# Kernel optimization log

Hardware: AMD Instinct MI355X
Metric: run time of the kernel (lower is better)

## Reference

```python
import math
import jax, jax.numpy as jnp
import numpy as np

S, B, H, D = 2048, 1, 16, 128  # seq, batch, heads, head_dim (hard-coded in source)
COEFF = 1.0  # layer_num = 1
NORM_FACTOR = math.sqrt(2048 / 16) * COEFF  # sqrt(HIDDEN/NUM_HEADS) * coeff


def setup_inputs() -> dict:
    key = jax.random.key(0)
    k1, k2, k3, k4, k5 = jax.random.split(key, 5)
    query_layer = jax.random.normal(k1, (S, B, H, D), dtype=jnp.float32)
    key_layer = jax.random.normal(k2, (S, B, H, D), dtype=jnp.float32)
    value_layer = jax.random.normal(k3, (S, B, H, D), dtype=jnp.float32)
    # causal mask, True = masked (Megatron convention)
    attention_mask = jnp.triu(jnp.ones((S, S), dtype=bool), k=1)[None, None]
    # per-head SVD right-singular-vector matrices (orthonormal-ish; random here)
    svd_qk = jax.random.normal(k4, (H, D, D), dtype=jnp.float32) / math.sqrt(D)
    svd_v = jax.random.normal(k5, (H, D, D), dtype=jnp.float32) / math.sqrt(D)
    return {"query_layer": query_layer, "key_layer": key_layer,
            "value_layer": value_layer, "attention_mask": attention_mask,
            "svd_qk": svd_qk, "svd_v": svd_v}


def reference(query_layer, key_layer, value_layer, attention_mask, svd_qk, svd_v):
    # q/k/v: [S, 1, H, D] -> project each head through its SVD matrix
    q = jnp.einsum('shd,hde->hse', query_layer[:, 0], svd_qk)  # [H,S,D]
    k = jnp.einsum('shd,hde->hse', key_layer[:, 0], svd_qk)    # [H,S,D]
    # qk_drop = 0 -> h_mask zeroing of columns is a no-op (faithfully skipped)
    scores = jnp.einsum('hqe,hke->hqk', q, k) / NORM_FACTOR    # [H,S,S]
    mask = attention_mask[0, 0]                                 # [S,S] bool
    scores = jnp.where(mask, jnp.float32(-10000.0), scores)
    # FusedScaleMaskSoftmax: scale by coeff, re-mask, softmax
    scaled = jnp.where(mask, jnp.float32(-10000.0), scores * COEFF)
    probs = jax.nn.softmax(scaled, axis=-1)                     # [H,S,S]
    # attention dropout is identity in eval mode
    v = jnp.einsum('shd,hde->hse', value_layer[:, 0], svd_v)    # [H,S,D]
    # vlinear_drop = 0 -> column zeroing is a no-op
    ctx = jnp.einsum('hqk,hke->qhe', probs, v)                  # [S,H,D]
    return ctx.reshape(S, B, H * D)                             # [S,1,2048]
```

## Files before the change

kernel.cpp:

```cpp
#include <hip/hip_runtime.h>
#include <hip/hip_bf16.h>
#include <math.h>

#define S_LEN 2048
#define NHEAD 16
#define DHEAD 128

typedef __attribute__((ext_vector_type(8)))  _Float16 f16x8;
typedef __attribute__((ext_vector_type(4)))  _Float16 f16x4;
typedef __attribute__((ext_vector_type(2)))  _Float16 f16x2;
typedef __attribute__((ext_vector_type(4)))  float    f32x4;
typedef __attribute__((ext_vector_type(16))) float    f32x16;

__device__ __forceinline__ void permswap(unsigned &a, unsigned &b) {
    asm volatile("v_permlane32_swap_b32 %0, %1" : "+v"(a), "+v"(b));
}

__global__ __launch_bounds__(256) void transpose_w_kernel(
    const float* __restrict__ w_qk, const float* __restrict__ w_v,
    _Float16* __restrict__ wqk_t, _Float16* __restrict__ wv_t)
{
    __shared__ float tile[32][33];
    const int mat = blockIdx.z;
    const int h   = blockIdx.y;
    const int t0  = blockIdx.x;
    const int dt  = (t0 >> 2) * 32;
    const int et  = (t0 & 3) * 32;
    const float* src = (mat ? w_v : w_qk) + (size_t)h * DHEAD * DHEAD;
    _Float16*   dst = (mat ? wv_t : wqk_t) + (size_t)h * DHEAD * DHEAD;
    const int tx = threadIdx.x & 31, ty = threadIdx.x >> 5;
#pragma unroll
    for (int k = 0; k < 4; ++k)
        tile[ty + 8 * k][tx] = src[(size_t)(dt + ty + 8 * k) * DHEAD + et + tx];
    __syncthreads();
#pragma unroll
    for (int k = 0; k < 4; ++k)
        dst[(size_t)(et + ty + 8 * k) * DHEAD + dt + tx] = (_Float16)tile[tx][ty + 8 * k];
}

__global__ __launch_bounds__(256) void proj_kernel(
    const float* __restrict__ q_in, const float* __restrict__ k_in,
    const float* __restrict__ v_in,
    const _Float16* __restrict__ wqk_t, const _Float16* __restrict__ wv_t,
    _Float16* __restrict__ Qp, _Float16* __restrict__ Kp, _Float16* __restrict__ Vt)
{
    const int h   = blockIdx.x >> 5;
    const int rb  = blockIdx.x & 31;
    const int wv  = threadIdx.x >> 6;
    const int lane = threadIdx.x & 63;
    const int r16 = lane & 15;
    const int kg  = lane >> 4;
    const int s_base = rb * 64 + wv * 16;
    const int s_row  = s_base + r16;
    const float INV_NORM = 0.08838834764831845f;

    f16x8 aq[4], ak[4], av[4];
    {
        const float* qr = q_in + ((size_t)s_row * NHEAD + h) * DHEAD;
        const float* kr = k_in + ((size_t)s_row * NHEAD + h) * DHEAD;
        const float* vr = v_in + ((size_t)s_row * NHEAD + h) * DHEAD;
#pragma unroll
        for (int kb = 0; kb < 4; ++kb) {
            const int d0 = kb * 32 + kg * 8;
            const f32x4 q0 = *(const f32x4*)(qr + d0), q1 = *(const f32x4*)(qr + d0 + 4);
            const f32x4 k0 = *(const f32x4*)(kr + d0), k1 = *(const f32x4*)(kr + d0 + 4);
            const f32x4 v0 = *(const f32x4*)(vr + d0), v1 = *(const f32x4*)(vr + d0 + 4);
#pragma unroll
            for (int i = 0; i < 4; ++i) {
                aq[kb][i] = (_Float16)q0[i];  aq[kb][i + 4] = (_Float16)q1[i];
                ak[kb][i] = (_Float16)k0[i];  ak[kb][i + 4] = (_Float16)k1[i];
                av[kb][i] = (_Float16)v0[i];  av[kb][i + 4] = (_Float16)v1[i];
            }
        }
    }

    const _Float16* wq_h = wqk_t + (size_t)h * DHEAD * DHEAD;
    const _Float16* wv_h = wv_t  + (size_t)h * DHEAD * DHEAD;

#pragma unroll 2
    for (int cb = 0; cb < 8; ++cb) {
        f32x4 accq = {0.f, 0.f, 0.f, 0.f};
        f32x4 acck = {0.f, 0.f, 0.f, 0.f};
        f32x4 accv = {0.f, 0.f, 0.f, 0.f};
        const int c = cb * 16 + r16;
#pragma unroll
        for (int kb = 0; kb < 4; ++kb) {
            const f16x8 bqk = *(const f16x8*)(wq_h + (size_t)c * DHEAD + kb * 32 + kg * 8);
            const f16x8 bv  = *(const f16x8*)(wv_h + (size_t)c * DHEAD + kb * 32 + kg * 8);
            accq = __builtin_amdgcn_mfma_f32_16x16x32_f16(aq[kb], bqk, accq, 0, 0, 0);
            acck = __builtin_amdgcn_mfma_f32_16x16x32_f16(ak[kb], bqk, acck, 0, 0, 0);
            accv = __builtin_amdgcn_mfma_f32_16x16x32_f16(av[kb], bv,  accv, 0, 0, 0);
        }
#pragma unroll
        for (int j = 0; j < 4; ++j) {
            const int sr = s_base + kg * 4 + j;
            Qp[((size_t)h * S_LEN + sr) * DHEAD + c] = (_Float16)(accq[j] * INV_NORM);
            Kp[((size_t)h * S_LEN + sr) * DHEAD + c] = (_Float16)acck[j];
        }
        f16x4 vvv;
#pragma unroll
        for (int j = 0; j < 4; ++j) vvv[j] = (_Float16)accv[j];
        *(f16x4*)(Vt + ((size_t)h * DHEAD + c) * S_LEN + s_base + kg * 4) = vvv;
    }
}

__global__ __launch_bounds__(512, 2) void attn_kernel(
    const _Float16* __restrict__ Qp, const _Float16* __restrict__ Kp,
    const _Float16* __restrict__ Vt, float* __restrict__ out)
{
    __shared__ _Float16 obuf[4][32][132];
    __shared__ float    mlbuf[4][2][32];

    const int h    = blockIdx.y;
    const int w    = threadIdx.x >> 6;
    const int lane = threadIdx.x & 63;
    const int q    = lane & 31;
    const int hi   = lane >> 5;

    const int qsub = w & 1;
    const int role = (w >> 1) & 1;
    const int tsel = w >> 2;
    const int t    = tsel ? (31 - blockIdx.x) : blockIdx.x;
    const int pairid = qsub + tsel * 2;
    const int q0w  = t * 64 + qsub * 32;
    const int jmax = 2 * t + 1 + qsub;
    const int q_abs = q0w + q;

    const _Float16* qbase = Qp + ((size_t)h * S_LEN + q0w) * DHEAD;
    const _Float16* kbase = Kp + (size_t)h * S_LEN * DHEAD;
    const _Float16* vbase = Vt + (size_t)h * DHEAD * S_LEN;

    const int lqk = q * DHEAD + hi * 8;
    const int lv  = q * S_LEN + hi * 8;

    f16x8 qf[8];
#pragma unroll
    for (int m = 0; m < 8; ++m)
        qf[m] = *(const f16x8*)(qbase + lqk + m * 16);

    f32x16 acc[4];
#pragma unroll
    for (int e = 0; e < 4; ++e)
#pragma unroll
        for (int i = 0; i < 16; ++i) acc[e][i] = 0.f;

    float m_run = -1e30f, l_run = 0.f;

    for (int j = role; j < jmax; j += 2) {
        const int kv0 = j * 32;

        const _Float16* kp = kbase + (size_t)kv0 * DHEAD + lqk;
        f16x8 kf[8];
#pragma unroll
        for (int m = 0; m < 8; ++m)
            kf[m] = *(const f16x8*)(kp + m * 16);

        f32x16 s0, s1;
#pragma unroll
        for (int i = 0; i < 16; ++i) { s0[i] = 0.f; s1[i] = 0.f; }
#pragma unroll
        for (int m = 0; m < 8; m += 2) {
            s0 = __builtin_amdgcn_mfma_f32_32x32x16_f16(kf[m],     qf[m],     s0, 0, 0, 0);
            s1 = __builtin_amdgcn_mfma_f32_32x32x16_f16(kf[m + 1], qf[m + 1], s1, 0, 0, 0);
        }

        f16x8 vf[8];
#pragma unroll
        for (int e = 0; e < 4; ++e) {
            const _Float16* vp = vbase + (size_t)e * 32 * S_LEN + lv + kv0;
            vf[2 * e]     = *(const f16x8*)(vp);
            vf[2 * e + 1] = *(const f16x8*)(vp + 16);
        }

        f32x16 sv = s0 + s1;

        if (kv0 == q0w) {
#pragma unroll
            for (int i = 0; i < 16; ++i) {
                const int krel = (i & 3) + 8 * (i >> 2) + 4 * hi;
                if (kv0 + krel > q_abs) sv[i] = -1e30f;
            }
        }

        float t0 = fmaxf(sv[0], sv[1]),  t1 = fmaxf(sv[2], sv[3]);
        float t2 = fmaxf(sv[4], sv[5]),  t3 = fmaxf(sv[6], sv[7]);
        float t4 = fmaxf(sv[8], sv[9]),  t5 = fmaxf(sv[10], sv[11]);
        float t6 = fmaxf(sv[12], sv[13]), t7 = fmaxf(sv[14], sv[15]);
        t0 = fmaxf(t0, t1); t2 = fmaxf(t2, t3); t4 = fmaxf(t4, t5); t6 = fmaxf(t6, t7);
        float tm = fmaxf(fmaxf(t0, t2), fmaxf(t4, t6));
        tm = fmaxf(tm, __shfl_xor(tm, 32, 64));

        const float mnew = fmaxf(m_run, tm);
        if (__any(tm > m_run)) {
            const float corr = __expf(m_run - mnew);
            l_run *= corr;
#pragma unroll
            for (int e = 0; e < 4; ++e)
#pragma unroll
                for (int i = 0; i < 16; ++i) acc[e][i] *= corr;
            m_run = mnew;
        }

#pragma unroll
        for (int i = 0; i < 16; ++i) sv[i] = __expf(sv[i] - m_run);
        float r0 = (sv[0] + sv[1]) + (sv[2] + sv[3]);
        float r1 = (sv[4] + sv[5]) + (sv[6] + sv[7]);
        float r2 = (sv[8] + sv[9]) + (sv[10] + sv[11]);
        float r3 = (sv[12] + sv[13]) + (sv[14] + sv[15]);
        float rs = (r0 + r1) + (r2 + r3);
        rs += __shfl_xor(rs, 32, 64);
        l_run += rs;

        unsigned u0 = __builtin_bit_cast(unsigned, __builtin_amdgcn_cvt_pkrtz(sv[0],  sv[1]));
        unsigned u1 = __builtin_bit_cast(unsigned, __builtin_amdgcn_cvt_pkrtz(sv[2],  sv[3]));
        unsigned u2 = __builtin_bit_cast(unsigned, __builtin_amdgcn_cvt_pkrtz(sv[4],  sv[5]));
        unsigned u3 = __builtin_bit_cast(unsigned, __builtin_amdgcn_cvt_pkrtz(sv[6],  sv[7]));
        unsigned u4 = __builtin_bit_cast(unsigned, __builtin_amdgcn_cvt_pkrtz(sv[8],  sv[9]));
        unsigned u5 = __builtin_bit_cast(unsigned, __builtin_amdgcn_cvt_pkrtz(sv[10], sv[11]));
        unsigned u6 = __builtin_bit_cast(unsigned, __builtin_amdgcn_cvt_pkrtz(sv[12], sv[13]));
        unsigned u7 = __builtin_bit_cast(unsigned, __builtin_amdgcn_cvt_pkrtz(sv[14], sv[15]));
        permswap(u0, u2); permswap(u1, u3);
        permswap(u4, u6); permswap(u5, u7);
        union uf8 { unsigned w[4]; f16x8 v; };
        uf8 p0; p0.w[0] = u0; p0.w[1] = u1; p0.w[2] = u2; p0.w[3] = u3;
        uf8 p1; p1.w[0] = u4; p1.w[1] = u5; p1.w[2] = u6; p1.w[3] = u7;

#pragma unroll
        for (int e = 0; e < 4; ++e) {
            acc[e] = __builtin_amdgcn_mfma_f32_32x32x16_f16(vf[2 * e],     p0.v, acc[e], 0, 0, 0);
            acc[e] = __builtin_amdgcn_mfma_f32_32x32x16_f16(vf[2 * e + 1], p1.v, acc[e], 0, 0, 0);
        }
    }

    if (role) {
        if (hi == 0) { mlbuf[pairid][0][q] = m_run; mlbuf[pairid][1][q] = l_run; }
#pragma unroll
        for (int e = 0; e < 4; ++e)
#pragma unroll
            for (int i = 0; i < 16; ++i) {
                const int erow = e * 32 + (i & 3) + 8 * (i >> 2) + 4 * hi;
                obuf[pairid][q][erow] = (_Float16)acc[e][i];
            }
    }
    __syncthreads();
    if (!role) {
        const float mb = mlbuf[pairid][0][q];
        const float lb = mlbuf[pairid][1][q];
        const float ms = fmaxf(m_run, mb);
        const float ca = __expf(m_run - ms);
        const float cb = __expf(mb - ms);
        const float rinv = 1.0f / (l_run * ca + lb * cb);
        float* orow = out + (size_t)q_abs * (NHEAD * DHEAD) + h * DHEAD;
#pragma unroll
        for (int e = 0; e < 4; ++e) {
#pragma unroll
            for (int g = 0; g < 4; ++g) {
                f32x4 vv;
#pragma unroll
                for (int c = 0; c < 4; ++c) {
                    const int i = g * 4 + c;
                    const int erow = e * 32 + 8 * g + 4 * hi + c;
                    vv[c] = (acc[e][i] * ca + (float)obuf[pairid][q][erow] * cb) * rinv;
                }
                *(f32x4*)(orow + e * 32 + 8 * g + 4 * hi) = vv;
            }
        }
    }
}

extern "C" void kernel_launch(void* const* d_in, const int* in_sizes, int n_in,
                              void* d_out, int out_size, void* d_ws, size_t ws_size,
                              hipStream_t stream) {
    const float* q_in = (const float*)d_in[0];
    const float* k_in = (const float*)d_in[1];
    const float* v_in = (const float*)d_in[2];
    const float* w_qk = (const float*)d_in[4];
    const float* w_v  = (const float*)d_in[5];
    float* out = (float*)d_out;

    const size_t mat_elems = (size_t)NHEAD * S_LEN * DHEAD;
    const size_t w_elems   = (size_t)NHEAD * DHEAD * DHEAD;
    _Float16* Qp   = (_Float16*)d_ws;
    _Float16* Kp   = Qp + mat_elems;
    _Float16* Vt   = Kp + mat_elems;
    _Float16* Wqkt = Vt + mat_elems;
    _Float16* Wvt  = Wqkt + w_elems;

    transpose_w_kernel<<<dim3(16, NHEAD, 2), dim3(256), 0, stream>>>(w_qk, w_v, Wqkt, Wvt);
    proj_kernel<<<dim3(NHEAD * 32), dim3(256), 0, stream>>>(q_in, k_in, v_in, Wqkt, Wvt, Qp, Kp, Vt);
    attn_kernel<<<dim3(16, NHEAD), dim3(512), 0, stream>>>(Qp, Kp, Vt, out);
}
```

Baseline: 105.0 us.

## Restructure attention into 16-row query tiles using 16x16x32 MFMA and K prefetch

```diff
diff --git a/kernel.cpp b/kernel.cpp
--- a/kernel.cpp
+++ b/kernel.cpp
@@ -8,13 +8,7 @@
 
 typedef __attribute__((ext_vector_type(8)))  _Float16 f16x8;
 typedef __attribute__((ext_vector_type(4)))  _Float16 f16x4;
-typedef __attribute__((ext_vector_type(2)))  _Float16 f16x2;
 typedef __attribute__((ext_vector_type(4)))  float    f32x4;
-typedef __attribute__((ext_vector_type(16))) float    f32x16;
-
-__device__ __forceinline__ void permswap(unsigned &a, unsigned &b) {
-    asm volatile("v_permlane32_swap_b32 %0, %1" : "+v"(a), "+v"(b));
-}
 
 __global__ __launch_bounds__(256) void transpose_w_kernel(
     const float* __restrict__ w_qk, const float* __restrict__ w_v,
@@ -52,7 +46,7 @@
     const int kg  = lane >> 4;
     const int s_base = rb * 64 + wv * 16;
     const int s_row  = s_base + r16;
-    const float INV_NORM = 0.08838834764831845f;
+    const float INV_NORM = 0.12752211758f;
 
     f16x8 aq[4], ak[4], av[4];
     {
@@ -104,166 +98,157 @@
     }
 }
 
-__global__ __launch_bounds__(512, 2) void attn_kernel(
+__global__ __launch_bounds__(512, 4) void attn_kernel(
     const _Float16* __restrict__ Qp, const _Float16* __restrict__ Kp,
     const _Float16* __restrict__ Vt, float* __restrict__ out)
 {
-    __shared__ _Float16 obuf[4][32][132];
-    __shared__ float    mlbuf[4][2][32];
+    __shared__ _Float16 obuf[4][16][136];
+    __shared__ float    mlbuf[4][2][16];
 
     const int h    = blockIdx.y;
     const int w    = threadIdx.x >> 6;
     const int lane = threadIdx.x & 63;
-    const int q    = lane & 31;
-    const int hi   = lane >> 5;
-
-    const int qsub = w & 1;
-    const int role = (w >> 1) & 1;
+    const int r16  = lane & 15;
+    const int kg   = lane >> 4;
+
     const int tsel = w >> 2;
-    const int t    = tsel ? (31 - blockIdx.x) : blockIdx.x;
-    const int pairid = qsub + tsel * 2;
-    const int q0w  = t * 64 + qsub * 32;
-    const int jmax = 2 * t + 1 + qsub;
-    const int q_abs = q0w + q;
-
-    const _Float16* qbase = Qp + ((size_t)h * S_LEN + q0w) * DHEAD;
+    const int qsub = (w >> 1) & 1;
+    const int role = w & 1;
+    const int t    = tsel ? (63 - blockIdx.x) : blockIdx.x;
+    const int mg   = tsel * 2 + qsub;
+    const int q0w  = t * 32 + qsub * 16;
+    const int jmax = t + 1;
+    const int q_abs = q0w + r16;
+
     const _Float16* kbase = Kp + (size_t)h * S_LEN * DHEAD;
     const _Float16* vbase = Vt + (size_t)h * DHEAD * S_LEN;
 
-    const int lqk = q * DHEAD + hi * 8;
-    const int lv  = q * S_LEN + hi * 8;
-
-    f16x8 qf[8];
-#pragma unroll
-    for (int m = 0; m < 8; ++m)
-        qf[m] = *(const f16x8*)(qbase + lqk + m * 16);
-
-    f32x16 acc[4];
-#pragma unroll
-    for (int e = 0; e < 4; ++e)
-#pragma unroll
-        for (int i = 0; i < 16; ++i) acc[e][i] = 0.f;
-
+    f16x8 qf[4];
+    {
+        const _Float16* qp = Qp + ((size_t)h * S_LEN + q_abs) * DHEAD + kg * 8;
+#pragma unroll
+        for (int st = 0; st < 4; ++st) qf[st] = *(const f16x8*)(qp + st * 32);
+    }
+
+    f32x4 acc[8];
+#pragma unroll
+    for (int eb = 0; eb < 8; ++eb) acc[eb] = (f32x4){0.f, 0.f, 0.f, 0.f};
     float m_run = -1e30f, l_run = 0.f;
 
-    for (int j = role; j < jmax; j += 2) {
+    const int lkoff = r16 * DHEAD + kg * 8;
+
+    auto loadK = [&](f16x8* kf, int j) {
+        const _Float16* kp = kbase + (size_t)(j * 32) * DHEAD + lkoff;
+#pragma unroll
+        for (int b = 0; b < 2; ++b)
+#pragma unroll
+            for (int st = 0; st < 4; ++st)
+                kf[b * 4 + st] = *(const f16x8*)(kp + b * 16 * DHEAD + st * 32);
+    };
+
+    auto tile = [&](const f16x8* kf, int j) {
         const int kv0 = j * 32;
-
-        const _Float16* kp = kbase + (size_t)kv0 * DHEAD + lqk;
-        f16x8 kf[8];
-#pragma unroll
-        for (int m = 0; m < 8; ++m)
-            kf[m] = *(const f16x8*)(kp + m * 16);
-
-        f32x16 s0, s1;
-#pragma unroll
-        for (int i = 0; i < 16; ++i) { s0[i] = 0.f; s1[i] = 0.f; }
-#pragma unroll
-        for (int m = 0; m < 8; m += 2) {
-            s0 = __builtin_amdgcn_mfma_f32_32x32x16_f16(kf[m],     qf[m],     s0, 0, 0, 0);
-            s1 = __builtin_amdgcn_mfma_f32_32x32x16_f16(kf[m + 1], qf[m + 1], s1, 0, 0, 0);
-        }
-
+        f32x4 s0 = {0.f, 0.f, 0.f, 0.f}, s1 = {0.f, 0.f, 0.f, 0.f};
+#pragma unroll
+        for (int st = 0; st < 4; ++st) {
+            s0 = __builtin_amdgcn_mfma_f32_16x16x32_f16(kf[st],     qf[st], s0, 0, 0, 0);
+            s1 = __builtin_amdgcn_mfma_f32_16x16x32_f16(kf[4 + st], qf[st], s1, 0, 0, 0);
+        }
         f16x8 vf[8];
 #pragma unroll
-        for (int e = 0; e < 4; ++e) {
-            const _Float16* vp = vbase + (size_t)e * 32 * S_LEN + lv + kv0;
-            vf[2 * e]     = *(const f16x8*)(vp);
-            vf[2 * e + 1] = *(const f16x8*)(vp + 16);
-        }
-
-        f32x16 sv = s0 + s1;
-
-        if (kv0 == q0w) {
-#pragma unroll
-            for (int i = 0; i < 16; ++i) {
-                const int krel = (i & 3) + 8 * (i >> 2) + 4 * hi;
+        for (int eb = 0; eb < 8; ++eb) {
+            const _Float16* vp = vbase + (size_t)(eb * 16 + r16) * S_LEN + kv0 + kg * 4;
+            union { f16x4 h[2]; f16x8 v; } uu;
+            uu.h[0] = *(const f16x4*)(vp);
+            uu.h[1] = *(const f16x4*)(vp + 16);
+            vf[eb] = uu.v;
+        }
+
+        float sv[8];
+#pragma unroll
+        for (int i = 0; i < 4; ++i) { sv[i] = s0[i]; sv[4 + i] = s1[i]; }
+
+        if (j == t) {
+#pragma unroll
+            for (int i = 0; i < 8; ++i) {
+                const int krel = ((i >> 2) << 4) + kg * 4 + (i & 3);
                 if (kv0 + krel > q_abs) sv[i] = -1e30f;
             }
         }
 
-        float t0 = fmaxf(sv[0], sv[1]),  t1 = fmaxf(sv[2], sv[3]);
-        float t2 = fmaxf(sv[4], sv[5]),  t3 = fmaxf(sv[6], sv[7]);
-        float t4 = fmaxf(sv[8], sv[9]),  t5 = fmaxf(sv[10], sv[11]);
-        float t6 = fmaxf(sv[12], sv[13]), t7 = fmaxf(sv[14], sv[15]);
-        t0 = fmaxf(t0, t1); t2 = fmaxf(t2, t3); t4 = fmaxf(t4, t5); t6 = fmaxf(t6, t7);
-        float tm = fmaxf(fmaxf(t0, t2), fmaxf(t4, t6));
+        float t0 = fmaxf(sv[0], sv[1]), t1 = fmaxf(sv[2], sv[3]);
+        float t2 = fmaxf(sv[4], sv[5]), t3 = fmaxf(sv[6], sv[7]);
+        float tm = fmaxf(fmaxf(t0, t1), fmaxf(t2, t3));
+        tm = fmaxf(tm, __shfl_xor(tm, 16, 64));
         tm = fmaxf(tm, __shfl_xor(tm, 32, 64));
-
-        const float mnew = fmaxf(m_run, tm);
         if (__any(tm > m_run)) {
-            const float corr = __expf(m_run - mnew);
+            const float mnew = fmaxf(m_run, tm);
+            const float corr = exp2f(m_run - mnew);
             l_run *= corr;
 #pragma unroll
-            for (int e = 0; e < 4; ++e)
-#pragma unroll
-                for (int i = 0; i < 16; ++i) acc[e][i] *= corr;
+            for (int eb = 0; eb < 8; ++eb)
+#pragma unroll
+                for (int jj = 0; jj < 4; ++jj) acc[eb][jj] *= corr;
             m_run = mnew;
         }
-
-#pragma unroll
-        for (int i = 0; i < 16; ++i) sv[i] = __expf(sv[i] - m_run);
-        float r0 = (sv[0] + sv[1]) + (sv[2] + sv[3]);
-        float r1 = (sv[4] + sv[5]) + (sv[6] + sv[7]);
-        float r2 = (sv[8] + sv[9]) + (sv[10] + sv[11]);
-        float r3 = (sv[12] + sv[13]) + (sv[14] + sv[15]);
-        float rs = (r0 + r1) + (r2 + r3);
+#pragma unroll
+        for (int i = 0; i < 8; ++i) sv[i] = exp2f(sv[i] - m_run);
+        float rs = ((sv[0] + sv[1]) + (sv[2] + sv[3])) + ((sv[4] + sv[5]) + (sv[6] + sv[7]));
+        rs += __shfl_xor(rs, 16, 64);
         rs += __shfl_xor(rs, 32, 64);
         l_run += rs;
 
-        unsigned u0 = __builtin_bit_cast(unsigned, __builtin_amdgcn_cvt_pkrtz(sv[0],  sv[1]));
-        unsigned u1 = __builtin_bit_cast(unsigned, __builtin_amdgcn_cvt_pkrtz(sv[2],  sv[3]));
-        unsigned u2 = __builtin_bit_cast(unsigned, __builtin_amdgcn_cvt_pkrtz(sv[4],  sv[5]));
-        unsigned u3 = __builtin_bit_cast(unsigned, __builtin_amdgcn_cvt_pkrtz(sv[6],  sv[7]));
-        unsigned u4 = __builtin_bit_cast(unsigned, __builtin_amdgcn_cvt_pkrtz(sv[8],  sv[9]));
-        unsigned u5 = __builtin_bit_cast(unsigned, __builtin_amdgcn_cvt_pkrtz(sv[10], sv[11]));
-        unsigned u6 = __builtin_bit_cast(unsigned, __builtin_amdgcn_cvt_pkrtz(sv[12], sv[13]));
-        unsigned u7 = __builtin_bit_cast(unsigned, __builtin_amdgcn_cvt_pkrtz(sv[14], sv[15]));
-        permswap(u0, u2); permswap(u1, u3);
-        permswap(u4, u6); permswap(u5, u7);
-        union uf8 { unsigned w[4]; f16x8 v; };
-        uf8 p0; p0.w[0] = u0; p0.w[1] = u1; p0.w[2] = u2; p0.w[3] = u3;
-        uf8 p1; p1.w[0] = u4; p1.w[1] = u5; p1.w[2] = u6; p1.w[3] = u7;
-
-#pragma unroll
-        for (int e = 0; e < 4; ++e) {
-            acc[e] = __builtin_amdgcn_mfma_f32_32x32x16_f16(vf[2 * e],     p0.v, acc[e], 0, 0, 0);
-            acc[e] = __builtin_amdgcn_mfma_f32_32x32x16_f16(vf[2 * e + 1], p1.v, acc[e], 0, 0, 0);
-        }
+        union uf8 { unsigned w[4]; f16x8 v; } pb;
+        pb.w[0] = __builtin_bit_cast(unsigned, __builtin_amdgcn_cvt_pkrtz(sv[0], sv[1]));
+        pb.w[1] = __builtin_bit_cast(unsigned, __builtin_amdgcn_cvt_pkrtz(sv[2], sv[3]));
+        pb.w[2] = __builtin_bit_cast(unsigned, __builtin_amdgcn_cvt_pkrtz(sv[4], sv[5]));
+        pb.w[3] = __builtin_bit_cast(unsigned, __builtin_amdgcn_cvt_pkrtz(sv[6], sv[7]));
+
+#pragma unroll
+        for (int eb = 0; eb < 8; ++eb)
+            acc[eb] = __builtin_amdgcn_mfma_f32_16x16x32_f16(vf[eb], pb.v, acc[eb], 0, 0, 0);
+    };
+
+    f16x8 ka[8], kb[8];
+    int j = role;
+    if (j < jmax) loadK(ka, j);
+    while (j < jmax) {
+        if (j + 2 < jmax) loadK(kb, j + 2);
+        tile(ka, j);
+        j += 2;
+        if (j >= jmax) break;
+        if (j + 2 < jmax) loadK(ka, j + 2);
+        tile(kb, j);
+        j += 2;
     }
 
     if (role) {
-        if (hi == 0) { mlbuf[pairid][0][q] = m_run; mlbuf[pairid][1][q] = l_run; }
-#pragma unroll
-        for (int e = 0; e < 4; ++e)
-#pragma unroll
-            for (int i = 0; i < 16; ++i) {
-                const int erow = e * 32 + (i & 3) + 8 * (i >> 2) + 4 * hi;
-                obuf[pairid][q][erow] = (_Float16)acc[e][i];
-            }
+        if (kg == 0) { mlbuf[mg][0][r16] = m_run; mlbuf[mg][1][r16] = l_run; }
+#pragma unroll
+        for (int eb = 0; eb < 8; ++eb) {
+            f16x4 ob;
+#pragma unroll
+            for (int jj = 0; jj < 4; ++jj) ob[jj] = (_Float16)acc[eb][jj];
+            *(f16x4*)&obuf[mg][r16][eb * 16 + kg * 4] = ob;
+        }
     }
     __syncthreads();
     if (!role) {
-        const float mb = mlbuf[pairid][0][q];
-        const float lb = mlbuf[pairid][1][q];
+        const float mb = mlbuf[mg][0][r16];
+        const float lb = mlbuf[mg][1][r16];
         const float ms = fmaxf(m_run, mb);
-        const float ca = __expf(m_run - ms);
-        const float cb = __expf(mb - ms);
+        const float ca = exp2f(m_run - ms);
+        const float cb = exp2f(mb - ms);
         const float rinv = 1.0f / (l_run * ca + lb * cb);
         float* orow = out + (size_t)q_abs * (NHEAD * DHEAD) + h * DHEAD;
 #pragma unroll
-        for (int e = 0; e < 4; ++e) {
-#pragma unroll
-            for (int g = 0; g < 4; ++g) {
-                f32x4 vv;
-#pragma unroll
-                for (int c = 0; c < 4; ++c) {
-                    const int i = g * 4 + c;
-                    const int erow = e * 32 + 8 * g + 4 * hi + c;
-                    vv[c] = (acc[e][i] * ca + (float)obuf[pairid][q][erow] * cb) * rinv;
-                }
-                *(f32x4*)(orow + e * 32 + 8 * g + 4 * hi) = vv;
-            }
+        for (int eb = 0; eb < 8; ++eb) {
+            const f16x4 ob = *(const f16x4*)&obuf[mg][r16][eb * 16 + kg * 4];
+            f32x4 vv;
+#pragma unroll
+            for (int jj = 0; jj < 4; ++jj)
+                vv[jj] = (acc[eb][jj] * ca + (float)ob[jj] * cb) * rinv;
+            *(f32x4*)(orow + eb * 16 + kg * 4) = vv;
         }
     }
 }
@@ -288,5 +273,5 @@
 
     transpose_w_kernel<<<dim3(16, NHEAD, 2), dim3(256), 0, stream>>>(w_qk, w_v, Wqkt, Wvt);
     proj_kernel<<<dim3(NHEAD * 32), dim3(256), 0, stream>>>(q_in, k_in, v_in, Wqkt, Wvt, Qp, Kp, Vt);
-    attn_kernel<<<dim3(16, NHEAD), dim3(512), 0, stream>>>(Qp, Kp, Vt, out);
-}
+    attn_kernel<<<dim3(32, NHEAD), dim3(512), 0, stream>>>(Qp, Kp, Vt, out);
+}
```

After: 372.2 us. 3.54x slower.

## Split KV loop four ways per query tile and vectorize projection stores

Applied to the files above, without the earlier changes.

```diff
diff --git a/kernel.cpp b/kernel.cpp
--- a/kernel.cpp
+++ b/kernel.cpp
@@ -8,7 +8,6 @@
 
 typedef __attribute__((ext_vector_type(8)))  _Float16 f16x8;
 typedef __attribute__((ext_vector_type(4)))  _Float16 f16x4;
-typedef __attribute__((ext_vector_type(2)))  _Float16 f16x2;
 typedef __attribute__((ext_vector_type(4)))  float    f32x4;
 typedef __attribute__((ext_vector_type(16))) float    f32x16;
 
@@ -87,41 +86,42 @@
         for (int kb = 0; kb < 4; ++kb) {
             const f16x8 bqk = *(const f16x8*)(wq_h + (size_t)c * DHEAD + kb * 32 + kg * 8);
             const f16x8 bv  = *(const f16x8*)(wv_h + (size_t)c * DHEAD + kb * 32 + kg * 8);
-            accq = __builtin_amdgcn_mfma_f32_16x16x32_f16(aq[kb], bqk, accq, 0, 0, 0);
-            acck = __builtin_amdgcn_mfma_f32_16x16x32_f16(ak[kb], bqk, acck, 0, 0, 0);
+            accq = __builtin_amdgcn_mfma_f32_16x16x32_f16(bqk, aq[kb], accq, 0, 0, 0);
+            acck = __builtin_amdgcn_mfma_f32_16x16x32_f16(bqk, ak[kb], acck, 0, 0, 0);
             accv = __builtin_amdgcn_mfma_f32_16x16x32_f16(av[kb], bv,  accv, 0, 0, 0);
         }
-#pragma unroll
-        for (int j = 0; j < 4; ++j) {
-            const int sr = s_base + kg * 4 + j;
-            Qp[((size_t)h * S_LEN + sr) * DHEAD + c] = (_Float16)(accq[j] * INV_NORM);
-            Kp[((size_t)h * S_LEN + sr) * DHEAD + c] = (_Float16)acck[j];
-        }
+        f16x4 qv, kv4;
+#pragma unroll
+        for (int jj = 0; jj < 4; ++jj) {
+            qv[jj]  = (_Float16)(accq[jj] * INV_NORM);
+            kv4[jj] = (_Float16)acck[jj];
+        }
+        *(f16x4*)(Qp + ((size_t)h * S_LEN + s_base + r16) * DHEAD + cb * 16 + kg * 4) = qv;
+        *(f16x4*)(Kp + ((size_t)h * S_LEN + s_base + r16) * DHEAD + cb * 16 + kg * 4) = kv4;
         f16x4 vvv;
 #pragma unroll
-        for (int j = 0; j < 4; ++j) vvv[j] = (_Float16)accv[j];
+        for (int jj = 0; jj < 4; ++jj) vvv[jj] = (_Float16)accv[jj];
         *(f16x4*)(Vt + ((size_t)h * DHEAD + c) * S_LEN + s_base + kg * 4) = vvv;
     }
 }
 
-__global__ __launch_bounds__(512, 2) void attn_kernel(
+__global__ __launch_bounds__(512, 4) void attn_kernel(
     const _Float16* __restrict__ Qp, const _Float16* __restrict__ Kp,
     const _Float16* __restrict__ Vt, float* __restrict__ out)
 {
-    __shared__ _Float16 obuf[4][32][132];
-    __shared__ float    mlbuf[4][2][32];
+    __shared__ _Float16 obuf[2][3][32][132];
+    __shared__ float    mlbuf[2][3][2][32];
 
     const int h    = blockIdx.y;
+    const int qsub = blockIdx.z;
     const int w    = threadIdx.x >> 6;
     const int lane = threadIdx.x & 63;
     const int q    = lane & 31;
     const int hi   = lane >> 5;
 
-    const int qsub = w & 1;
-    const int role = (w >> 1) & 1;
     const int tsel = w >> 2;
+    const int role = w & 3;
     const int t    = tsel ? (31 - blockIdx.x) : blockIdx.x;
-    const int pairid = qsub + tsel * 2;
     const int q0w  = t * 64 + qsub * 32;
     const int jmax = 2 * t + 1 + qsub;
     const int q_abs = q0w + q;
@@ -146,7 +146,7 @@
 
     float m_run = -1e30f, l_run = 0.f;
 
-    for (int j = role; j < jmax; j += 2) {
+    for (int j = role; j < jmax; j += 4) {
         const int kv0 = j * 32;
 
         const _Float16* kp = kbase + (size_t)kv0 * DHEAD + lqk;
@@ -232,24 +232,30 @@
         }
     }
 
-    if (role) {
-        if (hi == 0) { mlbuf[pairid][0][q] = m_run; mlbuf[pairid][1][q] = l_run; }
+    if (role != 0) {
+        if (hi == 0) {
+            mlbuf[tsel][role - 1][0][q] = m_run;
+            mlbuf[tsel][role - 1][1][q] = l_run;
+        }
 #pragma unroll
         for (int e = 0; e < 4; ++e)
 #pragma unroll
             for (int i = 0; i < 16; ++i) {
                 const int erow = e * 32 + (i & 3) + 8 * (i >> 2) + 4 * hi;
-                obuf[pairid][q][erow] = (_Float16)acc[e][i];
+                obuf[tsel][role - 1][q][erow] = (_Float16)acc[e][i];
             }
     }
     __syncthreads();
-    if (!role) {
-        const float mb = mlbuf[pairid][0][q];
-        const float lb = mlbuf[pairid][1][q];
-        const float ms = fmaxf(m_run, mb);
-        const float ca = __expf(m_run - ms);
-        const float cb = __expf(mb - ms);
-        const float rinv = 1.0f / (l_run * ca + lb * cb);
+    if (role == 0) {
+        const float m1 = mlbuf[tsel][0][0][q], l1 = mlbuf[tsel][0][1][q];
+        const float m2 = mlbuf[tsel][1][0][q], l2 = mlbuf[tsel][1][1][q];
+        const float m3 = mlbuf[tsel][2][0][q], l3 = mlbuf[tsel][2][1][q];
+        const float ms = fmaxf(fmaxf(m_run, m1), fmaxf(m2, m3));
+        const float c0 = __expf(m_run - ms);
+        const float c1 = __expf(m1 - ms);
+        const float c2 = __expf(m2 - ms);
+        const float c3 = __expf(m3 - ms);
+        const float rinv = 1.0f / (l_run * c0 + l1 * c1 + l2 * c2 + l3 * c3);
         float* orow = out + (size_t)q_abs * (NHEAD * DHEAD) + h * DHEAD;
 #pragma unroll
         for (int e = 0; e < 4; ++e) {
@@ -260,7 +266,10 @@
                 for (int c = 0; c < 4; ++c) {
                     const int i = g * 4 + c;
                     const int erow = e * 32 + 8 * g + 4 * hi + c;
-                    vv[c] = (acc[e][i] * ca + (float)obuf[pairid][q][erow] * cb) * rinv;
+                    vv[c] = (acc[e][i] * c0
+                             + (float)obuf[tsel][0][q][erow] * c1
+                             + (float)obuf[tsel][1][q][erow] * c2
+                             + (float)obuf[tsel][2][q][erow] * c3) * rinv;
                 }
                 *(f32x4*)(orow + e * 32 + 8 * g + 4 * hi) = vv;
             }
@@ -288,5 +297,5 @@
 
     transpose_w_kernel<<<dim3(16, NHEAD, 2), dim3(256), 0, stream>>>(w_qk, w_v, Wqkt, Wvt);
     proj_kernel<<<dim3(NHEAD * 32), dim3(256), 0, stream>>>(q_in, k_in, v_in, Wqkt, Wvt, Qp, Kp, Vt);
-    attn_kernel<<<dim3(16, NHEAD), dim3(512), 0, stream>>>(Qp, Kp, Vt, out);
-}
+    attn_kernel<<<dim3(16, NHEAD, 2), dim3(512), 0, stream>>>(Qp, Kp, Vt, out);
+}
```

After: 184.3 us. 75.5% more time.

## Stage K tiles through swizzled LDS with async global-to-LDS double buffering

Applied to the files above, without the earlier changes.

```diff
diff --git a/kernel.cpp b/kernel.cpp
--- a/kernel.cpp
+++ b/kernel.cpp
@@ -8,12 +8,17 @@
 
 typedef __attribute__((ext_vector_type(8)))  _Float16 f16x8;
 typedef __attribute__((ext_vector_type(4)))  _Float16 f16x4;
-typedef __attribute__((ext_vector_type(2)))  _Float16 f16x2;
 typedef __attribute__((ext_vector_type(4)))  float    f32x4;
 typedef __attribute__((ext_vector_type(16))) float    f32x16;
 
 __device__ __forceinline__ void permswap(unsigned &a, unsigned &b) {
     asm volatile("v_permlane32_swap_b32 %0, %1" : "+v"(a), "+v"(b));
+}
+
+typedef __attribute__((address_space(3))) unsigned int lds_u32;
+typedef __attribute__((address_space(1))) const unsigned int glb_u32;
+__device__ __forceinline__ void gload16(const void* g, void* l) {
+    __builtin_amdgcn_global_load_lds((glb_u32*)g, (lds_u32*)l, 16, 0, 0);
 }
 
 __global__ __launch_bounds__(256) void transpose_w_kernel(
@@ -87,20 +92,42 @@
         for (int kb = 0; kb < 4; ++kb) {
             const f16x8 bqk = *(const f16x8*)(wq_h + (size_t)c * DHEAD + kb * 32 + kg * 8);
             const f16x8 bv  = *(const f16x8*)(wv_h + (size_t)c * DHEAD + kb * 32 + kg * 8);
-            accq = __builtin_amdgcn_mfma_f32_16x16x32_f16(aq[kb], bqk, accq, 0, 0, 0);
-            acck = __builtin_amdgcn_mfma_f32_16x16x32_f16(ak[kb], bqk, acck, 0, 0, 0);
+            accq = __builtin_amdgcn_mfma_f32_16x16x32_f16(bqk, aq[kb], accq, 0, 0, 0);
+            acck = __builtin_amdgcn_mfma_f32_16x16x32_f16(bqk, ak[kb], acck, 0, 0, 0);
             accv = __builtin_amdgcn_mfma_f32_16x16x32_f16(av[kb], bv,  accv, 0, 0, 0);
         }
-#pragma unroll
-        for (int j = 0; j < 4; ++j) {
-            const int sr = s_base + kg * 4 + j;
-            Qp[((size_t)h * S_LEN + sr) * DHEAD + c] = (_Float16)(accq[j] * INV_NORM);
-            Kp[((size_t)h * S_LEN + sr) * DHEAD + c] = (_Float16)acck[j];
-        }
+        f16x4 qv, kv4;
+#pragma unroll
+        for (int jj = 0; jj < 4; ++jj) {
+            qv[jj]  = (_Float16)(accq[jj] * INV_NORM);
+            kv4[jj] = (_Float16)acck[jj];
+        }
+        *(f16x4*)(Qp + ((size_t)h * S_LEN + s_base + r16) * DHEAD + cb * 16 + kg * 4) = qv;
+        *(f16x4*)(Kp + ((size_t)h * S_LEN + s_base + r16) * DHEAD + cb * 16 + kg * 4) = kv4;
         f16x4 vvv;
 #pragma unroll
-        for (int j = 0; j < 4; ++j) vvv[j] = (_Float16)accv[j];
+        for (int jj = 0; jj < 4; ++jj) vvv[jj] = (_Float16)accv[jj];
         *(f16x4*)(Vt + ((size_t)h * DHEAD + c) * S_LEN + s_base + kg * 4) = vvv;
+    }
+}
+
+__device__ __forceinline__ void stage_k(const _Float16* kbase, _Float16* kst,
+                                        int w, int lane, int par, int inext,
+                                        int jmax_lock) {
+#pragma unroll
+    for (int cidx = 0; cidx < 2; ++cidx) {
+        const int c      = 2 * w + cidx;
+        const int role_c = c >> 3;
+        const int cc     = c & 7;
+        const int jn     = 2 * inext + role_c;
+        if (jn < jmax_lock) {
+            const int A    = cc * 1024 + lane * 16;
+            const int srcO = A ^ (((A >> 8) & 15) << 4);
+            const char* g  = (const char*)kbase + (size_t)jn * 8192 + srcO;
+            char*       l  = (char*)kst + (size_t)(role_c * 2 + par) * 8192
+                                        + cc * 1024;
+            gload16(g, l);
+        }
     }
 }
 
@@ -108,6 +135,7 @@
     const _Float16* __restrict__ Qp, const _Float16* __restrict__ Kp,
     const _Float16* __restrict__ Vt, float* __restrict__ out)
 {
+    __shared__ _Float16 Kst[4][4096];
     __shared__ _Float16 obuf[4][32][132];
     __shared__ float    mlbuf[4][2][32];
 
@@ -126,12 +154,16 @@
     const int jmax = 2 * t + 1 + qsub;
     const int q_abs = q0w + q;
 
+    const int jmax_lock = 2 * (31 - blockIdx.x) + 2;
+    const int I         = jmax_lock / 2;
+
     const _Float16* qbase = Qp + ((size_t)h * S_LEN + q0w) * DHEAD;
     const _Float16* kbase = Kp + (size_t)h * S_LEN * DHEAD;
     const _Float16* vbase = Vt + (size_t)h * DHEAD * S_LEN;
 
     const int lqk = q * DHEAD + hi * 8;
     const int lv  = q * S_LEN + hi * 8;
+    const int swq = (q & 15) << 4;
 
     f16x8 qf[8];
 #pragma unroll
@@ -146,89 +178,105 @@
 
     float m_run = -1e30f, l_run = 0.f;
 
-    for (int j = role; j < jmax; j += 2) {
+    stage_k(kbase, &Kst[0][0], w, lane, 0, 0, jmax_lock);
+
+    int p = 0;
+    for (int it = 0; it < I; ++it, p ^= 1) {
+        __syncthreads();
+
+        const int j   = 2 * it + role;
+        const bool act = (j < jmax);
         const int kv0 = j * 32;
 
-        const _Float16* kp = kbase + (size_t)kv0 * DHEAD + lqk;
         f16x8 kf[8];
-#pragma unroll
-        for (int m = 0; m < 8; ++m)
-            kf[m] = *(const f16x8*)(kp + m * 16);
-
-        f32x16 s0, s1;
-#pragma unroll
-        for (int i = 0; i < 16; ++i) { s0[i] = 0.f; s1[i] = 0.f; }
-#pragma unroll
-        for (int m = 0; m < 8; m += 2) {
-            s0 = __builtin_amdgcn_mfma_f32_32x32x16_f16(kf[m],     qf[m],     s0, 0, 0, 0);
-            s1 = __builtin_amdgcn_mfma_f32_32x32x16_f16(kf[m + 1], qf[m + 1], s1, 0, 0, 0);
-        }
-
-        f16x8 vf[8];
-#pragma unroll
-        for (int e = 0; e < 4; ++e) {
-            const _Float16* vp = vbase + (size_t)e * 32 * S_LEN + lv + kv0;
-            vf[2 * e]     = *(const f16x8*)(vp);
-            vf[2 * e + 1] = *(const f16x8*)(vp + 16);
-        }
-
-        f32x16 sv = s0 + s1;
-
-        if (kv0 == q0w) {
-#pragma unroll
-            for (int i = 0; i < 16; ++i) {
-                const int krel = (i & 3) + 8 * (i >> 2) + 4 * hi;
-                if (kv0 + krel > q_abs) sv[i] = -1e30f;
-            }
-        }
-
-        float t0 = fmaxf(sv[0], sv[1]),  t1 = fmaxf(sv[2], sv[3]);
-        float t2 = fmaxf(sv[4], sv[5]),  t3 = fmaxf(sv[6], sv[7]);
-        float t4 = fmaxf(sv[8], sv[9]),  t5 = fmaxf(sv[10], sv[11]);
-        float t6 = fmaxf(sv[12], sv[13]), t7 = fmaxf(sv[14], sv[15]);
-        t0 = fmaxf(t0, t1); t2 = fmaxf(t2, t3); t4 = fmaxf(t4, t5); t6 = fmaxf(t6, t7);
-        float tm = fmaxf(fmaxf(t0, t2), fmaxf(t4, t6));
-        tm = fmaxf(tm, __shfl_xor(tm, 32, 64));
-
-        const float mnew = fmaxf(m_run, tm);
-        if (__any(tm > m_run)) {
-            const float corr = __expf(m_run - mnew);
-            l_run *= corr;
-#pragma unroll
-            for (int e = 0; e < 4; ++e)
-#pragma unroll
-                for (int i = 0; i < 16; ++i) acc[e][i] *= corr;
-            m_run = mnew;
-        }
-
-#pragma unroll
-        for (int i = 0; i < 16; ++i) sv[i] = __expf(sv[i] - m_run);
-        float r0 = (sv[0] + sv[1]) + (sv[2] + sv[3]);
-        float r1 = (sv[4] + sv[5]) + (sv[6] + sv[7]);
-        float r2 = (sv[8] + sv[9]) + (sv[10] + sv[11]);
-        float r3 = (sv[12] + sv[13]) + (sv[14] + sv[15]);
-        float rs = (r0 + r1) + (r2 + r3);
-        rs += __shfl_xor(rs, 32, 64);
-        l_run += rs;
-
-        unsigned u0 = __builtin_bit_cast(unsigned, __builtin_amdgcn_cvt_pkrtz(sv[0],  sv[1]));
-        unsigned u1 = __builtin_bit_cast(unsigned, __builtin_amdgcn_cvt_pkrtz(sv[2],  sv[3]));
-        unsigned u2 = __builtin_bit_cast(unsigned, __builtin_amdgcn_cvt_pkrtz(sv[4],  sv[5]));
-        unsigned u3 = __builtin_bit_cast(unsigned, __builtin_amdgcn_cvt_pkrtz(sv[6],  sv[7]));
-        unsigned u4 = __builtin_bit_cast(unsigned, __builtin_amdgcn_cvt_pkrtz(sv[8],  sv[9]));
-        unsigned u5 = __builtin_bit_cast(unsigned, __builtin_amdgcn_cvt_pkrtz(sv[10], sv[11]));
-        unsigned u6 = __builtin_bit_cast(unsigned, __builtin_amdgcn_cvt_pkrtz(sv[12], sv[13]));
-        unsigned u7 = __builtin_bit_cast(unsigned, __builtin_amdgcn_cvt_pkrtz(sv[14], sv[15]));
-        permswap(u0, u2); permswap(u1, u3);
-        permswap(u4, u6); permswap(u5, u7);
-        union uf8 { unsigned w[4]; f16x8 v; };
-        uf8 p0; p0.w[0] = u0; p0.w[1] = u1; p0.w[2] = u2; p0.w[3] = u3;
-        uf8 p1; p1.w[0] = u4; p1.w[1] = u5; p1.w[2] = u6; p1.w[3] = u7;
-
-#pragma unroll
-        for (int e = 0; e < 4; ++e) {
-            acc[e] = __builtin_amdgcn_mfma_f32_32x32x16_f16(vf[2 * e],     p0.v, acc[e], 0, 0, 0);
-            acc[e] = __builtin_amdgcn_mfma_f32_32x32x16_f16(vf[2 * e + 1], p1.v, acc[e], 0, 0, 0);
+        if (act) {
+            const char* kt = (const char*)&Kst[role * 2 + p][0];
+#pragma unroll
+            for (int m = 0; m < 8; ++m) {
+                const int L = q * 256 + m * 32 + hi * 16;
+                kf[m] = *(const f16x8*)(kt + (L ^ swq));
+            }
+        }
+
+        if (it + 1 < I)
+            stage_k(kbase, &Kst[0][0], w, lane, p ^ 1, it + 1, jmax_lock);
+
+        if (act) {
+            f32x16 s0, s1;
+#pragma unroll
+            for (int i = 0; i < 16; ++i) { s0[i] = 0.f; s1[i] = 0.f; }
+#pragma unroll
+            for (int m = 0; m < 8; m += 2) {
+                s0 = __builtin_amdgcn_mfma_f32_32x32x16_f16(kf[m],     qf[m],     s0, 0, 0, 0);
+                s1 = __builtin_amdgcn_mfma_f32_32x32x16_f16(kf[m + 1], qf[m + 1], s1, 0, 0, 0);
+            }
+
+            f16x8 vf[8];
+#pragma unroll
+            for (int e = 0; e < 4; ++e) {
+                const _Float16* vp = vbase + (size_t)e * 32 * S_LEN + lv + kv0;
+                vf[2 * e]     = *(const f16x8*)(vp);
+                vf[2 * e + 1] = *(const f16x8*)(vp + 16);
+            }
+
+            f32x16 sv = s0 + s1;
+
+            if (kv0 == q0w) {
+#pragma unroll
+                for (int i = 0; i < 16; ++i) {
+                    const int krel = (i & 3) + 8 * (i >> 2) + 4 * hi;
+                    if (kv0 + krel > q_abs) sv[i] = -1e30f;
+                }
+            }
+
+            float t0 = fmaxf(sv[0], sv[1]),  t1 = fmaxf(sv[2], sv[3]);
+            float t2 = fmaxf(sv[4], sv[5]),  t3 = fmaxf(sv[6], sv[7]);
+            float t4 = fmaxf(sv[8], sv[9]),  t5 = fmaxf(sv[10], sv[11]);
+            float t6 = fmaxf(sv[12], sv[13]), t7 = fmaxf(sv[14], sv[15]);
+            t0 = fmaxf(t0, t1); t2 = fmaxf(t2, t3); t4 = fmaxf(t4, t5); t6 = fmaxf(t6, t7);
+            float tm = fmaxf(fmaxf(t0, t2), fmaxf(t4, t6));
+            tm = fmaxf(tm, __shfl_xor(tm, 32, 64));
+
+            const float mnew = fmaxf(m_run, tm);
+            if (__any(tm > m_run)) {
+                const float corr = __expf(m_run - mnew);
+                l_run *= corr;
+#pragma unroll
+                for (int e = 0; e < 4; ++e)
+#pragma unroll
+                    for (int i = 0; i < 16; ++i) acc[e][i] *= corr;
+                m_run = mnew;
+            }
+
+#pragma unroll
+            for (int i = 0; i < 16; ++i) sv[i] = __expf(sv[i] - m_run);
+            float r0 = (sv[0] + sv[1]) + (sv[2] + sv[3]);
+            float r1 = (sv[4] + sv[5]) + (sv[6] + sv[7]);
+            float r2 = (sv[8] + sv[9]) + (sv[10] + sv[11]);
+            float r3 = (sv[12] + sv[13]) + (sv[14] + sv[15]);
+            float rs = (r0 + r1) + (r2 + r3);
+            rs += __shfl_xor(rs, 32, 64);
+            l_run += rs;
+
+            unsigned u0 = __builtin_bit_cast(unsigned, __builtin_amdgcn_cvt_pkrtz(sv[0],  sv[1]));
+            unsigned u1 = __builtin_bit_cast(unsigned, __builtin_amdgcn_cvt_pkrtz(sv[2],  sv[3]));
+            unsigned u2 = __builtin_bit_cast(unsigned, __builtin_amdgcn_cvt_pkrtz(sv[4],  sv[5]));
+            unsigned u3 = __builtin_bit_cast(unsigned, __builtin_amdgcn_cvt_pkrtz(sv[6],  sv[7]));
+            unsigned u4 = __builtin_bit_cast(unsigned, __builtin_amdgcn_cvt_pkrtz(sv[8],  sv[9]));
+            unsigned u5 = __builtin_bit_cast(unsigned, __builtin_amdgcn_cvt_pkrtz(sv[10], sv[11]));
+            unsigned u6 = __builtin_bit_cast(unsigned, __builtin_amdgcn_cvt_pkrtz(sv[12], sv[13]));
+            unsigned u7 = __builtin_bit_cast(unsigned, __builtin_amdgcn_cvt_pkrtz(sv[14], sv[15]));
+            permswap(u0, u2); permswap(u1, u3);
+            permswap(u4, u6); permswap(u5, u7);
+            union uf8 { unsigned w[4]; f16x8 v; };
+            uf8 p0; p0.w[0] = u0; p0.w[1] = u1; p0.w[2] = u2; p0.w[3] = u3;
+            uf8 p1; p1.w[0] = u4; p1.w[1] = u5; p1.w[2] = u6; p1.w[3] = u7;
+
+#pragma unroll
+            for (int e = 0; e < 4; ++e) {
+                acc[e] = __builtin_amdgcn_mfma_f32_32x32x16_f16(vf[2 * e],     p0.v, acc[e], 0, 0, 0);
+                acc[e] = __builtin_amdgcn_mfma_f32_32x32x16_f16(vf[2 * e + 1], p1.v, acc[e], 0, 0, 0);
+            }
         }
     }
 
```

Measured after the change: 92.44 us. -12.0%, faster.
